# Kernel optimization log

Measured on AMD Instinct MI355X. Metric: run time of the kernel, lower is better.

The kernel has to match this reference:

```python
import jax, jax.numpy as jnp
import numpy as np

N, NS, IN_P, OUT_P, SHARE = 65536, 16, 256, 256, 8
MID = OUT_P
EPS = 1e-5


def _bn(x, gamma, beta):
    # torch BatchNorm1d (training mode, biased var) applied over the channel
    # (last) axis; stats over all other axes. Matches BN on x.transpose(1,2).
    mean = x.mean(axis=(0, 1), keepdims=True)
    var = ((x - mean) ** 2).mean(axis=(0, 1), keepdims=True)
    return gamma * (x - mean) * jax.lax.rsqrt(var + EPS) + beta


def setup_inputs() -> dict:
    key = jax.random.key(0)
    ks = jax.random.split(key, 12)
    w = lambda k, shape: jax.random.normal(k, shape, dtype=jnp.float32) * 0.02
    return {
        "p": jax.random.uniform(ks[0], (N, 3), dtype=jnp.float32),
        "x": jax.random.normal(ks[1], (N, IN_P), dtype=jnp.float32),
        "idx": jax.random.randint(ks[2], (N, NS), 0, N),
        "wq": w(ks[3], (MID, IN_P)), "bq": jnp.zeros((MID,), jnp.float32),
        "wk": w(ks[4], (MID, IN_P)), "bk": jnp.zeros((MID,), jnp.float32),
        "wv": w(ks[5], (OUT_P, IN_P)), "bv": jnp.zeros((OUT_P,), jnp.float32),
        "wp1": w(ks[6], (3, 3)), "bp1": jnp.zeros((3,), jnp.float32),
        "gp": jnp.ones((3,), jnp.float32), "btp": jnp.zeros((3,), jnp.float32),
        "wp2": w(ks[7], (OUT_P, 3)), "bp2": jnp.zeros((OUT_P,), jnp.float32),
        "g1": jnp.ones((MID,), jnp.float32), "b1": jnp.zeros((MID,), jnp.float32),
        "ww1": w(ks[8], (MID // SHARE, MID)), "bw1": jnp.zeros((MID // SHARE,), jnp.float32),
        "g2": jnp.ones((MID // SHARE,), jnp.float32), "b2": jnp.zeros((MID // SHARE,), jnp.float32),
        "ww2": w(ks[9], (OUT_P // SHARE, OUT_P // SHARE)), "bw2": jnp.zeros((OUT_P // SHARE,), jnp.float32),
    }


def reference(p, x, idx, wq, bq, wk, bk, wv, bv, wp1, bp1, gp, btp, wp2, bp2,
              g1, b1, ww1, bw1, g2, b2, ww2, bw2):
    # q/k/v projections: [N, C]
    xq = x @ wq.T + bq
    xk = x @ wk.T + bk
    xv = x @ wv.T + bv
    # queryandgroup: gather neighbor features + relative positions
    xk_g = xk[idx]                      # [N, NS, MID]
    xv_g = xv[idx]                      # [N, NS, OUT_P]
    p_r = p[idx] - p[:, None, :]        # [N, NS, 3]  (use_xyz relative coords)
    # linear_p: Linear(3,3) -> BN(3) -> ReLU -> Linear(3, OUT_P)
    p_r = p_r @ wp1.T + bp1
    p_r = jax.nn.relu(_bn(p_r, gp, btp))
    p_r = p_r @ wp2.T + bp2             # [N, NS, OUT_P]
    # vector attention logits; out_planes // mid_planes == 1 so the
    # view(...).sum(2) of p_r is just p_r
    w = xk_g - xq[:, None, :] + p_r     # [N, NS, MID]
    # linear_w: BN -> ReLU -> Linear(MID, MID/S) -> BN -> ReLU -> Linear
    w = jax.nn.relu(_bn(w, g1, b1))
    w = w @ ww1.T + bw1                 # [N, NS, MID/S]
    w = jax.nn.relu(_bn(w, g2, b2))
    w = w @ ww2.T + bw2                 # [N, NS, OUT_P/S]
    w = jax.nn.softmax(w, axis=1)       # softmax over neighbors
    # grouped weighted sum with shared attention planes
    n, ns, c = xv_g.shape
    out = ((xv_g + p_r).reshape(n, ns, SHARE, c // SHARE)
           * w[:, :, None, :]).sum(axis=1).reshape(n, c)
    return out
```

## Files before the change

kernel.cpp:

```cpp
#include <hip/hip_runtime.h>
#include <hip/hip_bf16.h>

#define NPTS 65536
#define NSAMP 16
#define CH 256
#define CNT (NPTS * NSAMP)
#define EPSV 1e-5f

typedef __hip_bfloat16 bf16;
typedef __attribute__((ext_vector_type(8))) short short8;
typedef __attribute__((ext_vector_type(4))) short sh4;
typedef __attribute__((ext_vector_type(4))) float floatx4;

__device__ __forceinline__ float b2f(bf16 v) { return __bfloat162float(v); }

__device__ __forceinline__ float s2f(short v) {
    return __uint_as_float(((unsigned)(unsigned short)v) << 16);
}

__device__ __forceinline__ short f2bf_bits(float f) {
    bf16 h = __float2bfloat16(f);
    short s;
    __builtin_memcpy(&s, &h, 2);
    return s;
}

__global__ __launch_bounds__(256) void convw_kernel(
    const float* __restrict__ wq, const float* __restrict__ wk,
    const float* __restrict__ wv, const float* __restrict__ ww2,
    bf16* __restrict__ Wcat, bf16* __restrict__ ww2b)
{
    if (blockIdx.x < 96) {
        int e = (blockIdx.x * 256 + threadIdx.x) * 8;
        const float* src = (e < 65536) ? wq : (e < 131072) ? wk : wv;
        int off = e & 65535;
        float4 f0 = *(const float4*)(src + off);
        float4 f1 = *(const float4*)(src + off + 4);
        short8 r;
        r[0] = f2bf_bits(f0.x); r[1] = f2bf_bits(f0.y);
        r[2] = f2bf_bits(f0.z); r[3] = f2bf_bits(f0.w);
        r[4] = f2bf_bits(f1.x); r[5] = f2bf_bits(f1.y);
        r[6] = f2bf_bits(f1.z); r[7] = f2bf_bits(f1.w);
        *(short8*)(Wcat + e) = r;
    } else {
        int e = threadIdx.x * 4;
        float4 f = *(const float4*)(ww2 + e);
        sh4 r;
        r[0] = f2bf_bits(f.x); r[1] = f2bf_bits(f.y);
        r[2] = f2bf_bits(f.z); r[3] = f2bf_bits(f.w);
        *(sh4*)(ww2b + e) = r;
    }
}

__global__ __launch_bounds__(256) void gemm_kernel(
    const float* __restrict__ x, const bf16* __restrict__ Wcat,
    const float* __restrict__ bq, const float* __restrict__ bk,
    const float* __restrict__ bv,
    bf16* __restrict__ xq, bf16* __restrict__ xk, bf16* __restrict__ xv)
{
    __shared__ __align__(16) bf16 As[128 * 40];
    __shared__ __align__(16) bf16 Bs[128 * 40];

    int t = threadIdx.x, lane = t & 63, wave = t >> 6;
    int m0 = blockIdx.x * 128;
    int y = blockIdx.y, n0 = y * 128;
    int srow = t >> 1, sch = t & 1;
    int m = lane & 15, q = lane >> 4;
    int wm = wave >> 1, wn = wave & 1;

    floatx4 acc[4][4];
#pragma unroll
    for (int a = 0; a < 4; a++)
#pragma unroll
        for (int b = 0; b < 4; b++) acc[a][b] = (floatx4){0.f, 0.f, 0.f, 0.f};

    for (int kk = 0; kk < 256; kk += 32) {
        const float* ap = x + (size_t)(m0 + srow) * 256 + kk + sch * 16;
        float4 a0 = *(const float4*)(ap);
        float4 a1 = *(const float4*)(ap + 4);
        float4 a2 = *(const float4*)(ap + 8);
        float4 a3 = *(const float4*)(ap + 12);
        short8 h0, h1;
        h0[0] = f2bf_bits(a0.x); h0[1] = f2bf_bits(a0.y);
        h0[2] = f2bf_bits(a0.z); h0[3] = f2bf_bits(a0.w);
        h0[4] = f2bf_bits(a1.x); h0[5] = f2bf_bits(a1.y);
        h0[6] = f2bf_bits(a1.z); h0[7] = f2bf_bits(a1.w);
        h1[0] = f2bf_bits(a2.x); h1[1] = f2bf_bits(a2.y);
        h1[2] = f2bf_bits(a2.z); h1[3] = f2bf_bits(a2.w);
        h1[4] = f2bf_bits(a3.x); h1[5] = f2bf_bits(a3.y);
        h1[6] = f2bf_bits(a3.z); h1[7] = f2bf_bits(a3.w);
        *(short8*)&As[srow * 40 + sch * 16]     = h0;
        *(short8*)&As[srow * 40 + sch * 16 + 8] = h1;
        const bf16* bp = Wcat + (size_t)(n0 + srow) * 256 + kk + sch * 16;
        *(short8*)&Bs[srow * 40 + sch * 16]     = *(const short8*)bp;
        *(short8*)&Bs[srow * 40 + sch * 16 + 8] = *(const short8*)(bp + 8);
        __syncthreads();

        short8 av[4], bvv[4];
#pragma unroll
        for (int mt = 0; mt < 4; mt++)
            av[mt] = *(const short8*)&As[(wm * 64 + mt * 16 + m) * 40 + q * 8];
#pragma unroll
        for (int nt = 0; nt < 4; nt++)
            bvv[nt] = *(const short8*)&Bs[(wn * 64 + nt * 16 + m) * 40 + q * 8];
#pragma unroll
        for (int mt = 0; mt < 4; mt++)
#pragma unroll
            for (int nt = 0; nt < 4; nt++)
                acc[mt][nt] = __builtin_amdgcn_mfma_f32_16x16x32_bf16(av[mt], bvv[nt], acc[mt][nt], 0, 0, 0);
        __syncthreads();
    }

    int z = y >> 1;
    bf16* O        = (z == 0) ? xq : (z == 1) ? xk : xv;
    const float* B = (z == 0) ? bq : (z == 1) ? bk : bv;
    int cbase = (y & 1) * 128 + wn * 64;
#pragma unroll
    for (int nt = 0; nt < 4; nt++) {
        int oc = cbase + nt * 16 + m;
        float bias = B[oc];
#pragma unroll
        for (int mt = 0; mt < 4; mt++) {
            int grow = m0 + wm * 64 + mt * 16 + q * 4;
#pragma unroll
            for (int i = 0; i < 4; i++)
                O[(size_t)(grow + i) * 256 + oc] = __float2bfloat16(acc[mt][nt][i] + bias);
        }
    }
}

__global__ __launch_bounds__(256) void statsp_kernel(
    const float* __restrict__ p, const int* __restrict__ idx,
    const float* __restrict__ wp1, const float* __restrict__ bp1,
    float* __restrict__ statsP)
{
    float W00 = wp1[0], W01 = wp1[1], W02 = wp1[2];
    float W10 = wp1[3], W11 = wp1[4], W12 = wp1[5];
    float W20 = wp1[6], W21 = wp1[7], W22 = wp1[8];
    float B0 = bp1[0], B1 = bp1[1], B2 = bp1[2];

    float s0 = 0, s1 = 0, s2 = 0, q0 = 0, q1 = 0, q2 = 0;
    int stride = gridDim.x * blockDim.x;
    for (int r = blockIdx.x * blockDim.x + threadIdx.x; r < CNT; r += stride) {
        int n = r >> 4;
        int i = idx[r];
        float a0 = p[3 * (size_t)i]     - p[3 * (size_t)n];
        float a1 = p[3 * (size_t)i + 1] - p[3 * (size_t)n + 1];
        float a2 = p[3 * (size_t)i + 2] - p[3 * (size_t)n + 2];
        float v0 = W00 * a0 + W01 * a1 + W02 * a2 + B0;
        float v1 = W10 * a0 + W11 * a1 + W12 * a2 + B1;
        float v2 = W20 * a0 + W21 * a1 + W22 * a2 + B2;
        s0 += v0; q0 += v0 * v0;
        s1 += v1; q1 += v1 * v1;
        s2 += v2; q2 += v2 * v2;
    }
    float v[6] = {s0, s1, s2, q0, q1, q2};
#pragma unroll
    for (int k = 0; k < 6; k++) {
        float xv = v[k];
#pragma unroll
        for (int off = 32; off > 0; off >>= 1) xv += __shfl_down(xv, off);
        if ((threadIdx.x & 63) == 0) atomicAdd(&statsP[k], xv);
    }
}

__global__ void finalize_kernel(const float* __restrict__ stats,
                                const float* __restrict__ gamma,
                                const float* __restrict__ beta,
                                float* __restrict__ ss, int nch)
{
    int c = threadIdx.x;
    if (c < nch) {
        float inv = 1.0f / (float)CNT;
        float mean = stats[c] * inv;
        float var = stats[nch + c] * inv - mean * mean;
        float sc = gamma[c] * rsqrtf(var + EPSV);
        ss[c] = sc;
        ss[nch + c] = beta[c] - mean * sc;
    }
}

__global__ __launch_bounds__(256) void computer_kernel(
    const float* __restrict__ p, const int* __restrict__ idx,
    const float* __restrict__ wp1, const float* __restrict__ bp1,
    const float* __restrict__ ssP, float4* __restrict__ r4)
{
    float W00 = wp1[0], W01 = wp1[1], W02 = wp1[2];
    float W10 = wp1[3], W11 = wp1[4], W12 = wp1[5];
    float W20 = wp1[6], W21 = wp1[7], W22 = wp1[8];
    float B0 = bp1[0], B1 = bp1[1], B2 = bp1[2];
    float sc0 = ssP[0], sc1 = ssP[1], sc2 = ssP[2];
    float sh0 = ssP[3], sh1 = ssP[4], sh2 = ssP[5];

    int stride = gridDim.x * blockDim.x;
    for (int r = blockIdx.x * blockDim.x + threadIdx.x; r < CNT; r += stride) {
        int n = r >> 4;
        int i = idx[r];
        float a0 = p[3 * (size_t)i]     - p[3 * (size_t)n];
        float a1 = p[3 * (size_t)i + 1] - p[3 * (size_t)n + 1];
        float a2 = p[3 * (size_t)i + 2] - p[3 * (size_t)n + 2];
        float v0 = fmaxf(sc0 * (W00 * a0 + W01 * a1 + W02 * a2 + B0) + sh0, 0.f);
        float v1 = fmaxf(sc1 * (W10 * a0 + W11 * a1 + W12 * a2 + B1) + sh1, 0.f);
        float v2 = fmaxf(sc2 * (W20 * a0 + W21 * a1 + W22 * a2 + B2) + sh2, 0.f);
        r4[r] = make_float4(v0, v1, v2, 0.f);
    }
}

__global__ __launch_bounds__(256) void stats1_kernel(
    const int* __restrict__ idx, const float4* __restrict__ r4,
    const bf16* __restrict__ xk, const bf16* __restrict__ xq,
    const float* __restrict__ wp2, const float* __restrict__ bp2,
    float* __restrict__ stats1)
{
    __shared__ int idxs[1024];
    __shared__ float redS[8 * 264];
    __shared__ float redQ[8 * 264];

    int t = threadIdx.x;
    int r0 = blockIdx.x * 1024;
    for (int e = t; e < 1024; e += 256) idxs[e] = idx[r0 + e];

    int sub = t & 31, rl = t >> 5, cb = sub * 8;
    float w0[8], w1[8], w2[8], bc[8];
#pragma unroll
    for (int k = 0; k < 8; k++) {
        w0[k] = wp2[3 * (cb + k)];
        w1[k] = wp2[3 * (cb + k) + 1];
        w2[k] = wp2[3 * (cb + k) + 2];
        bc[k] = bp2[cb + k];
    }
    float s8[8] = {0, 0, 0, 0, 0, 0, 0, 0};
    float q8[8] = {0, 0, 0, 0, 0, 0, 0, 0};
    __syncthreads();

#pragma unroll 4
    for (int rr = rl; rr < 1024; rr += 8) {
        int r = r0 + rr;
        int i = idxs[rr];
        float4 rv = r4[r];
        short8 kv = *(const short8*)(xk + (size_t)i * 256 + cb);
        short8 qv = *(const short8*)(xq + (size_t)(r >> 4) * 256 + cb);
#pragma unroll
        for (int k = 0; k < 8; k++) {
            float w = s2f(kv[k]) - s2f(qv[k]) + rv.x * w0[k] + rv.y * w1[k] + rv.z * w2[k] + bc[k];
            s8[k] += w; q8[k] += w * w;
        }
    }
#pragma unroll
    for (int k = 0; k < 8; k++) {
        redS[rl * 264 + cb + k] = s8[k];
        redQ[rl * 264 + cb + k] = q8[k];
    }
    __syncthreads();
    int c = t;
    float ts = 0, tq = 0;
#pragma unroll
    for (int sr = 0; sr < 8; sr++) {
        ts += redS[sr * 264 + c];
        tq += redQ[sr * 264 + c];
    }
    atomicAdd(&stats1[c], ts);
    atomicAdd(&stats1[256 + c], tq);
}

__global__ __launch_bounds__(256) void stats2_kernel(
    const int* __restrict__ idx, const float4* __restrict__ r4,
    const bf16* __restrict__ xk, const bf16* __restrict__ xq,
    const float* __restrict__ wp2, const float* __restrict__ bp2,
    const float* __restrict__ ss1,
    const float* __restrict__ ww1, const float* __restrict__ bw1,
    bf16* __restrict__ y2, float* __restrict__ stats2)
{
    __shared__ __align__(16) bf16 hb[64 * 264];
    __shared__ __align__(16) bf16 ws1[32 * 264];
    __shared__ int idxs[1024];

    int t = threadIdx.x;
    int lane = t & 63, wave = t >> 6;
    int m = lane & 15, q = lane >> 4;
    int sub = t & 31, rl = t >> 5, cb = sub * 8;
    int r0 = blockIdx.x * 1024;

    for (int e = t; e < 8192; e += 256)
        ws1[(e >> 8) * 264 + (e & 255)] = __float2bfloat16(ww1[e]);
    for (int e = t; e < 1024; e += 256) idxs[e] = idx[r0 + e];

    float w0[8], w1[8], w2[8], bc[8], s1c[8], t1c[8];
#pragma unroll
    for (int k = 0; k < 8; k++) {
        w0[k] = wp2[3 * (cb + k)];
        w1[k] = wp2[3 * (cb + k) + 1];
        w2[k] = wp2[3 * (cb + k) + 2];
        bc[k] = bp2[cb + k];
        s1c[k] = ss1[cb + k];
        t1c[k] = ss1[256 + cb + k];
    }
    float bw0 = bw1[m], bw16 = bw1[16 + m];
    float jsum0 = 0, jsum1 = 0, jsq0 = 0, jsq1 = 0;
    __syncthreads();

    for (int it = 0; it < 16; it++) {
        int rb = r0 + it * 64;
#pragma unroll 2
        for (int rr = rl; rr < 64; rr += 8) {
            int r = rb + rr;
            int i = idxs[it * 64 + rr];
            float4 rv = r4[r];
            short8 kv = *(const short8*)(xk + (size_t)i * 256 + cb);
            short8 qv = *(const short8*)(xq + (size_t)(r >> 4) * 256 + cb);
            short8 h;
#pragma unroll
            for (int k = 0; k < 8; k++) {
                float w = s2f(kv[k]) - s2f(qv[k]) + rv.x * w0[k] + rv.y * w1[k] + rv.z * w2[k] + bc[k];
                h[k] = f2bf_bits(fmaxf(s1c[k] * w + t1c[k], 0.f));
            }
            *(short8*)&hb[rr * 264 + cb] = h;
        }
        __syncthreads();
        floatx4 a0 = (floatx4){0.f, 0.f, 0.f, 0.f};
        floatx4 a1 = (floatx4){0.f, 0.f, 0.f, 0.f};
        const bf16* abase = hb + (wave * 16 + m) * 264 + q * 8;
#pragma unroll
        for (int k = 0; k < 8; k++) {
            short8 af = *(const short8*)(abase + k * 32);
            short8 b0 = *(const short8*)&ws1[m * 264 + k * 32 + q * 8];
            short8 b1 = *(const short8*)&ws1[(16 + m) * 264 + k * 32 + q * 8];
            a0 = __builtin_amdgcn_mfma_f32_16x16x32_bf16(af, b0, a0, 0, 0, 0);
            a1 = __builtin_amdgcn_mfma_f32_16x16x32_bf16(af, b1, a1, 0, 0, 0);
        }
        int grow = rb + wave * 16 + q * 4;
#pragma unroll
        for (int ii = 0; ii < 4; ii++) {
            float y0 = a0[ii] + bw0;
            float y1 = a1[ii] + bw16;
            jsum0 += y0; jsq0 += y0 * y0;
            jsum1 += y1; jsq1 += y1 * y1;
            y2[(size_t)(grow + ii) * 32 + m]      = __float2bfloat16(y0);
            y2[(size_t)(grow + ii) * 32 + 16 + m] = __float2bfloat16(y1);
        }
        __syncthreads();
    }
    jsum0 += __shfl_xor(jsum0, 16); jsum0 += __shfl_xor(jsum0, 32);
    jsum1 += __shfl_xor(jsum1, 16); jsum1 += __shfl_xor(jsum1, 32);
    jsq0  += __shfl_xor(jsq0, 16);  jsq0  += __shfl_xor(jsq0, 32);
    jsq1  += __shfl_xor(jsq1, 16);  jsq1  += __shfl_xor(jsq1, 32);
    if (q == 0) {
        atomicAdd(&stats2[m], jsum0);
        atomicAdd(&stats2[16 + m], jsum1);
        atomicAdd(&stats2[32 + m], jsq0);
        atomicAdd(&stats2[48 + m], jsq1);
    }
}

__global__ __launch_bounds__(256) void final_kernel(
    const int* __restrict__ idx, const float4* __restrict__ r4,
    const bf16* __restrict__ xv,
    const float* __restrict__ wp2, const float* __restrict__ bp2,
    const bf16* __restrict__ y2, const float* __restrict__ ss2,
    const bf16* __restrict__ ww2b, const float* __restrict__ bw2,
    float* __restrict__ out)
{
    __shared__ __align__(16) float wsm[4][16][36];
    __shared__ float Asm[4][4][32];

    int t = threadIdx.x, wave = t >> 6, lane = t & 63;
    int m = lane & 15, q = lane >> 4;

    short8 bf0 = *(const short8*)(ww2b + m * 32 + q * 8);
    short8 bf1 = *(const short8*)(ww2b + (16 + m) * 32 + q * 8);
    float bwj0 = bw2[m], bwj1 = bw2[16 + m];

    float s2c[8], t2c[8];
#pragma unroll
    for (int k = 0; k < 8; k++) {
        s2c[k] = ss2[q * 8 + k];
        t2c[k] = ss2[32 + q * 8 + k];
    }

    int c0 = lane * 4;
    int j4 = (lane & 7) * 4;
    float wpc0[4], wpc1[4], wpc2[4], bpc[4];
#pragma unroll
    for (int k = 0; k < 4; k++) {
        wpc0[k] = wp2[(c0 + k) * 3];
        wpc1[k] = wp2[(c0 + k) * 3 + 1];
        wpc2[k] = wp2[(c0 + k) * 3 + 2];
        bpc[k]  = bp2[c0 + k];
    }

    int pbase = (blockIdx.x * 4 + wave) * 8;
    for (int pp = 0; pp < 8; pp++) {
        int n = pbase + pp;
        size_t rbase = (size_t)n * 16;

        int iv = idx[rbase + m];

        short8 yv = *(const short8*)(y2 + (rbase + m) * 32 + q * 8);
        short8 av;
#pragma unroll
        for (int k = 0; k < 8; k++)
            av[k] = f2bf_bits(fmaxf(s2c[k] * s2f(yv[k]) + t2c[k], 0.f));

        floatx4 l0 = (floatx4){bwj0, bwj0, bwj0, bwj0};
        floatx4 l1 = (floatx4){bwj1, bwj1, bwj1, bwj1};
        l0 = __builtin_amdgcn_mfma_f32_16x16x32_bf16(av, bf0, l0, 0, 0, 0);
        l1 = __builtin_amdgcn_mfma_f32_16x16x32_bf16(av, bf1, l1, 0, 0, 0);

        float mx0 = fmaxf(fmaxf(l0[0], l0[1]), fmaxf(l0[2], l0[3]));
        float mx1 = fmaxf(fmaxf(l1[0], l1[1]), fmaxf(l1[2], l1[3]));
        mx0 = fmaxf(mx0, __shfl_xor(mx0, 16));
        mx0 = fmaxf(mx0, __shfl_xor(mx0, 32));
        mx1 = fmaxf(mx1, __shfl_xor(mx1, 16));
        mx1 = fmaxf(mx1, __shfl_xor(mx1, 32));
        float w0[4], w1[4];
        float sum0 = 0.f, sum1 = 0.f;
#pragma unroll
        for (int i = 0; i < 4; i++) {
            w0[i] = __expf(l0[i] - mx0); sum0 += w0[i];
            w1[i] = __expf(l1[i] - mx1); sum1 += w1[i];
        }
        sum0 += __shfl_xor(sum0, 16); sum0 += __shfl_xor(sum0, 32);
        sum1 += __shfl_xor(sum1, 16); sum1 += __shfl_xor(sum1, 32);
        float inv0 = 1.f / sum0, inv1 = 1.f / sum1;

        float A00 = 0, A10 = 0, A20 = 0, A30 = 0;
        float A01 = 0, A11 = 0, A21 = 0, A31 = 0;
#pragma unroll
        for (int i = 0; i < 4; i++) {
            w0[i] *= inv0; w1[i] *= inv1;
            float4 rv = r4[rbase + q * 4 + i];
            A00 += rv.x * w0[i]; A10 += rv.y * w0[i];
            A20 += rv.z * w0[i]; A30 += w0[i];
            A01 += rv.x * w1[i]; A11 += rv.y * w1[i];
            A21 += rv.z * w1[i]; A31 += w1[i];
            wsm[wave][q * 4 + i][m]      = w0[i];
            wsm[wave][q * 4 + i][16 + m] = w1[i];
        }
        A00 += __shfl_xor(A00, 16); A00 += __shfl_xor(A00, 32);
        A10 += __shfl_xor(A10, 16); A10 += __shfl_xor(A10, 32);
        A20 += __shfl_xor(A20, 16); A20 += __shfl_xor(A20, 32);
        A30 += __shfl_xor(A30, 16); A30 += __shfl_xor(A30, 32);
        A01 += __shfl_xor(A01, 16); A01 += __shfl_xor(A01, 32);
        A11 += __shfl_xor(A11, 16); A11 += __shfl_xor(A11, 32);
        A21 += __shfl_xor(A21, 16); A21 += __shfl_xor(A21, 32);
        A31 += __shfl_xor(A31, 16); A31 += __shfl_xor(A31, 32);
        if (q == 0) {
            Asm[wave][0][m] = A00; Asm[wave][1][m] = A10;
            Asm[wave][2][m] = A20; Asm[wave][3][m] = A30;
            Asm[wave][0][16 + m] = A01; Asm[wave][1][16 + m] = A11;
            Asm[wave][2][16 + m] = A21; Asm[wave][3][16 + m] = A31;
        }

        float acc0 = 0, acc1 = 0, acc2 = 0, acc3 = 0;
#pragma unroll
        for (int s = 0; s < 16; s++) {
            int i = __builtin_amdgcn_readlane(iv, s);
            sh4 vv = *(const sh4*)(xv + (size_t)i * 256 + c0);
            float4 wv = *(const float4*)&wsm[wave][s][j4];
            acc0 += s2f(vv[0]) * wv.x;
            acc1 += s2f(vv[1]) * wv.y;
            acc2 += s2f(vv[2]) * wv.z;
            acc3 += s2f(vv[3]) * wv.w;
        }

        float res[4] = {acc0, acc1, acc2, acc3};
#pragma unroll
        for (int k = 0; k < 4; k++) {
            int j = j4 + k;
            res[k] += wpc0[k] * Asm[wave][0][j] + wpc1[k] * Asm[wave][1][j]
                    + wpc2[k] * Asm[wave][2][j] + bpc[k]  * Asm[wave][3][j];
        }
        *(float4*)(out + (size_t)n * 256 + c0) =
            make_float4(res[0], res[1], res[2], res[3]);
    }
}

extern "C" void kernel_launch(void* const* d_in, const int* in_sizes, int n_in,
                              void* d_out, int out_size, void* d_ws, size_t ws_size,
                              hipStream_t stream) {
    (void)in_sizes; (void)n_in; (void)out_size; (void)ws_size;

    const float* p   = (const float*)d_in[0];
    const float* x   = (const float*)d_in[1];
    const int*   idx = (const int*)d_in[2];
    const float* wq  = (const float*)d_in[3];  const float* bq  = (const float*)d_in[4];
    const float* wk  = (const float*)d_in[5];  const float* bk  = (const float*)d_in[6];
    const float* wv  = (const float*)d_in[7];  const float* bv  = (const float*)d_in[8];
    const float* wp1 = (const float*)d_in[9];  const float* bp1 = (const float*)d_in[10];
    const float* gp  = (const float*)d_in[11]; const float* btp = (const float*)d_in[12];
    const float* wp2 = (const float*)d_in[13]; const float* bp2 = (const float*)d_in[14];
    const float* g1  = (const float*)d_in[15]; const float* b1  = (const float*)d_in[16];
    const float* ww1 = (const float*)d_in[17]; const float* bw1 = (const float*)d_in[18];
    const float* g2  = (const float*)d_in[19]; const float* b2  = (const float*)d_in[20];
    const float* ww2 = (const float*)d_in[21]; const float* bw2 = (const float*)d_in[22];
    float* out = (float*)d_out;

    float* fws    = (float*)d_ws;
    float* statsP = fws;
    float* ssP    = fws + 8;
    float* stats1 = fws + 16;
    float* ss1    = fws + 528;
    float* stats2 = fws + 1040;
    float* ss2    = fws + 1104;
    bf16* ww2b = (bf16*)((char*)d_ws + 6144);
    bf16* Wcat = (bf16*)((char*)d_ws + 8192);
    bf16* xq = (bf16*)((char*)d_ws + 401408);
    bf16* xk = xq + (size_t)NPTS * CH;
    bf16* xv = xk + (size_t)NPTS * CH;
    bf16* y2 = xv + (size_t)NPTS * CH;
    float4* r4 = (float4*)(y2 + (size_t)CNT * 32);

    hipMemsetAsync(d_ws, 0, 8192, stream);

    convw_kernel<<<97, 256, 0, stream>>>(wq, wk, wv, ww2, Wcat, ww2b);
    gemm_kernel<<<dim3(512, 6), 256, 0, stream>>>(x, Wcat, bq, bk, bv, xq, xk, xv);
    statsp_kernel<<<512, 256, 0, stream>>>(p, idx, wp1, bp1, statsP);
    finalize_kernel<<<1, 256, 0, stream>>>(statsP, gp, btp, ssP, 3);
    computer_kernel<<<1024, 256, 0, stream>>>(p, idx, wp1, bp1, ssP, r4);
    stats1_kernel<<<1024, 256, 0, stream>>>(idx, r4, xk, xq, wp2, bp2, stats1);
    finalize_kernel<<<1, 256, 0, stream>>>(stats1, g1, b1, ss1, 256);
    stats2_kernel<<<1024, 256, 0, stream>>>(idx, r4, xk, xq, wp2, bp2, ss1, ww1, bw1, y2, stats2);
    finalize_kernel<<<1, 256, 0, stream>>>(stats2, g2, b2, ss2, 32);
    final_kernel<<<2048, 256, 0, stream>>>(idx, r4, xv, wp2, bp2, y2, ss2, ww2b, bw2, out);
}
```

Before: 801.5 us.

## Build MFMA A-fragments in registers directly, dropping LDS staging in stats2

The stats2 kernel now has each wave handle one point (16 neighbours) per iteration. It computes the BN1+ReLU activations directly in MFMA A-fragment layout in registers, so they are no longer written to shared memory and re-read. The ww1 weights are held as preloaded B-fragments in registers, and the per-channel scale/shift constants are folded into a small LDS table. Both block-level barriers inside the loop are removed and the grid is doubled. In exchange, register pressure goes up, and the gather reads become 16-byte per-lane accesses with less coalescing per row.

```diff
diff --git a/kernel.cpp b/kernel.cpp
--- a/kernel.cpp
+++ b/kernel.cpp
@@ -271,74 +271,89 @@
     const float* __restrict__ ww1, const float* __restrict__ bw1,
     bf16* __restrict__ y2, float* __restrict__ stats2)
 {
-    __shared__ __align__(16) bf16 hb[64 * 264];
-    __shared__ __align__(16) bf16 ws1[32 * 264];
-    __shared__ int idxs[1024];
-
-    int t = threadIdx.x;
-    int lane = t & 63, wave = t >> 6;
+    __shared__ __align__(16) float4 cA[288];
+    __shared__ float cB[288];
+
+    int t = threadIdx.x, lane = t & 63, wave = t >> 6;
     int m = lane & 15, q = lane >> 4;
-    int sub = t & 31, rl = t >> 5, cb = sub * 8;
-    int r0 = blockIdx.x * 1024;
-
-    for (int e = t; e < 8192; e += 256)
-        ws1[(e >> 8) * 264 + (e & 255)] = __float2bfloat16(ww1[e]);
-    for (int e = t; e < 1024; e += 256) idxs[e] = idx[r0 + e];
-
-    float w0[8], w1[8], w2[8], bc[8], s1c[8], t1c[8];
+
+    {
+        int c = t;
+        int k = c >> 5, qq = (c >> 3) & 3, j = c & 7;
+        float s1 = ss1[c], t1 = ss1[256 + c];
+        float4 v;
+        v.x = s1 * wp2[3 * c];
+        v.y = s1 * wp2[3 * c + 1];
+        v.z = s1 * wp2[3 * c + 2];
+        v.w = s1 * bp2[c] + t1;
+        cA[(k * 4 + qq) * 9 + j] = v;
+        cB[(k * 4 + qq) * 9 + j] = s1;
+    }
+
+    short8 bf0[8], bf1[8];
 #pragma unroll
     for (int k = 0; k < 8; k++) {
-        w0[k] = wp2[3 * (cb + k)];
-        w1[k] = wp2[3 * (cb + k) + 1];
-        w2[k] = wp2[3 * (cb + k) + 2];
-        bc[k] = bp2[cb + k];
-        s1c[k] = ss1[cb + k];
-        t1c[k] = ss1[256 + cb + k];
+        const float* w0p = ww1 + m * 256 + k * 32 + q * 8;
+        const float* w1p = ww1 + (16 + m) * 256 + k * 32 + q * 8;
+        float4 u0 = *(const float4*)(w0p);
+        float4 u1 = *(const float4*)(w0p + 4);
+        float4 u2 = *(const float4*)(w1p);
+        float4 u3 = *(const float4*)(w1p + 4);
+        short8 b0, b1;
+        b0[0] = f2bf_bits(u0.x); b0[1] = f2bf_bits(u0.y);
+        b0[2] = f2bf_bits(u0.z); b0[3] = f2bf_bits(u0.w);
+        b0[4] = f2bf_bits(u1.x); b0[5] = f2bf_bits(u1.y);
+        b0[6] = f2bf_bits(u1.z); b0[7] = f2bf_bits(u1.w);
+        b1[0] = f2bf_bits(u2.x); b1[1] = f2bf_bits(u2.y);
+        b1[2] = f2bf_bits(u2.z); b1[3] = f2bf_bits(u2.w);
+        b1[4] = f2bf_bits(u3.x); b1[5] = f2bf_bits(u3.y);
+        b1[6] = f2bf_bits(u3.z); b1[7] = f2bf_bits(u3.w);
+        bf0[k] = b0; bf1[k] = b1;
     }
     float bw0 = bw1[m], bw16 = bw1[16 + m];
+    __syncthreads();
+
     float jsum0 = 0, jsum1 = 0, jsq0 = 0, jsq1 = 0;
-    __syncthreads();
-
-    for (int it = 0; it < 16; it++) {
-        int rb = r0 + it * 64;
-#pragma unroll 2
-        for (int rr = rl; rr < 64; rr += 8) {
-            int r = rb + rr;
-            int i = idxs[it * 64 + rr];
-            float4 rv = r4[r];
-            short8 kv = *(const short8*)(xk + (size_t)i * 256 + cb);
-            short8 qv = *(const short8*)(xq + (size_t)(r >> 4) * 256 + cb);
-            short8 h;
-#pragma unroll
-            for (int k = 0; k < 8; k++) {
-                float w = s2f(kv[k]) - s2f(qv[k]) + rv.x * w0[k] + rv.y * w1[k] + rv.z * w2[k] + bc[k];
-                h[k] = f2bf_bits(fmaxf(s1c[k] * w + t1c[k], 0.f));
+    int pbase = (blockIdx.x * 4 + wave) * 8;
+    for (int pp = 0; pp < 8; pp++) {
+        int n = pbase + pp;
+        size_t rbase = (size_t)n * 16;
+        int iv = idx[rbase + m];
+        float4 rv = r4[rbase + m];
+        const bf16* kp = xk + (size_t)iv * 256 + q * 8;
+        const bf16* qp = xq + (size_t)n * 256 + q * 8;
+
+        short8 kvv[8];
+#pragma unroll
+        for (int k = 0; k < 8; k++)
+            kvv[k] = *(const short8*)(kp + k * 32);
+
+        floatx4 a0 = (floatx4){bw0, bw0, bw0, bw0};
+        floatx4 a1 = (floatx4){bw16, bw16, bw16, bw16};
+#pragma unroll
+        for (int k = 0; k < 8; k++) {
+            short8 qv = *(const short8*)(qp + k * 32);
+            int cb9 = (k * 4 + q) * 9;
+            short8 av;
+#pragma unroll
+            for (int j = 0; j < 8; j++) {
+                float4 cw = cA[cb9 + j];
+                float s1 = cB[cb9 + j];
+                float d = s2f(kvv[k][j]) - s2f(qv[j]);
+                float pr = fmaf(rv.x, cw.x, fmaf(rv.y, cw.y, fmaf(rv.z, cw.z, cw.w)));
+                av[j] = f2bf_bits(fmaxf(fmaf(s1, d, pr), 0.f));
             }
-            *(short8*)&hb[rr * 264 + cb] = h;
-        }
-        __syncthreads();
-        floatx4 a0 = (floatx4){0.f, 0.f, 0.f, 0.f};
-        floatx4 a1 = (floatx4){0.f, 0.f, 0.f, 0.f};
-        const bf16* abase = hb + (wave * 16 + m) * 264 + q * 8;
-#pragma unroll
-        for (int k = 0; k < 8; k++) {
-            short8 af = *(const short8*)(abase + k * 32);
-            short8 b0 = *(const short8*)&ws1[m * 264 + k * 32 + q * 8];
-            short8 b1 = *(const short8*)&ws1[(16 + m) * 264 + k * 32 + q * 8];
-            a0 = __builtin_amdgcn_mfma_f32_16x16x32_bf16(af, b0, a0, 0, 0, 0);
-            a1 = __builtin_amdgcn_mfma_f32_16x16x32_bf16(af, b1, a1, 0, 0, 0);
-        }
-        int grow = rb + wave * 16 + q * 4;
-#pragma unroll
-        for (int ii = 0; ii < 4; ii++) {
-            float y0 = a0[ii] + bw0;
-            float y1 = a1[ii] + bw16;
+            a0 = __builtin_amdgcn_mfma_f32_16x16x32_bf16(av, bf0[k], a0, 0, 0, 0);
+            a1 = __builtin_amdgcn_mfma_f32_16x16x32_bf16(av, bf1[k], a1, 0, 0, 0);
+        }
+#pragma unroll
+        for (int i = 0; i < 4; i++) {
+            float y0 = a0[i], y1 = a1[i];
             jsum0 += y0; jsq0 += y0 * y0;
             jsum1 += y1; jsq1 += y1 * y1;
-            y2[(size_t)(grow + ii) * 32 + m]      = __float2bfloat16(y0);
-            y2[(size_t)(grow + ii) * 32 + 16 + m] = __float2bfloat16(y1);
-        }
-        __syncthreads();
+            y2[(rbase + q * 4 + i) * 32 + m]      = __float2bfloat16(y0);
+            y2[(rbase + q * 4 + i) * 32 + 16 + m] = __float2bfloat16(y1);
+        }
     }
     jsum0 += __shfl_xor(jsum0, 16); jsum0 += __shfl_xor(jsum0, 32);
     jsum1 += __shfl_xor(jsum1, 16); jsum1 += __shfl_xor(jsum1, 32);
@@ -519,7 +534,7 @@
     computer_kernel<<<1024, 256, 0, stream>>>(p, idx, wp1, bp1, ssP, r4);
     stats1_kernel<<<1024, 256, 0, stream>>>(idx, r4, xk, xq, wp2, bp2, stats1);
     finalize_kernel<<<1, 256, 0, stream>>>(stats1, g1, b1, ss1, 256);
-    stats2_kernel<<<1024, 256, 0, stream>>>(idx, r4, xk, xq, wp2, bp2, ss1, ww1, bw1, y2, stats2);
+    stats2_kernel<<<2048, 256, 0, stream>>>(idx, r4, xk, xq, wp2, bp2, ss1, ww1, bw1, y2, stats2);
     finalize_kernel<<<1, 256, 0, stream>>>(stats2, g2, b2, ss2, 32);
     final_kernel<<<2048, 256, 0, stream>>>(idx, r4, xv, wp2, bp2, y2, ss2, ww2b, bw2, out);
 }
```

Measured after the change: 1.042 ms. 1.3x slower.
